# Kernel optimization log

Measured on AMD Instinct MI355X. Metric: run time of the kernel, lower is better.

Reference implementation:

```python
import jax, jax.numpy as jnp
from jax import lax
import numpy as np

D = 56      # latent_rep_size
H = 501     # GRU hidden size
T = 277     # repeat length (sequence length)
O = 76      # fc2 output


def setup_inputs() -> dict:
    key = jax.random.key(0)
    ks = jax.random.split(key, 20)
    B = 256
    s = 0.05
    inp = {"x": jax.random.normal(ks[0], (B, D), dtype=jnp.float32)}
    inp["fc1_w"] = jax.random.normal(ks[1], (D, D), dtype=jnp.float32) * s
    inp["fc1_b"] = jax.random.normal(ks[2], (D,), dtype=jnp.float32) * s
    k = 3
    for l, in_dim in enumerate([D, H, H]):
        inp[f"w_ih{l}"] = jax.random.normal(ks[k], (3 * H, in_dim), dtype=jnp.float32) * s; k += 1
        inp[f"w_hh{l}"] = jax.random.normal(ks[k], (3 * H, H), dtype=jnp.float32) * s; k += 1
        inp[f"b_ih{l}"] = jax.random.normal(ks[k], (3 * H,), dtype=jnp.float32) * s; k += 1
        inp[f"b_hh{l}"] = jax.random.normal(ks[k], (3 * H,), dtype=jnp.float32) * s; k += 1
    inp["fc2_w"] = jax.random.normal(ks[k], (O, H), dtype=jnp.float32) * s; k += 1
    inp["fc2_b"] = jax.random.normal(ks[k], (O,), dtype=jnp.float32) * s
    return inp


def _gru_step(h, g, w_hh, b_hh):
    # g: precomputed input gates (B, 3H) in PyTorch order [r, z, n]
    hg = h @ w_hh.T + b_hh                       # (B, 3H)
    r = jax.nn.sigmoid(g[:, :H] + hg[:, :H])
    z = jax.nn.sigmoid(g[:, H:2 * H] + hg[:, H:2 * H])
    n = jnp.tanh(g[:, 2 * H:] + r * hg[:, 2 * H:])
    h_new = (1.0 - z) * n + z * h
    return h_new, h_new


def _gru_layer(x_gates, w_hh, b_hh, B, dtype):
    # x_gates: (T, B, 3H) input contribution per timestep
    h0 = jnp.zeros((B, H), dtype)
    _, ys = lax.scan(lambda h, g: _gru_step(h, g, w_hh, b_hh), h0, x_gates)
    return ys  # (T, B, H)


def reference(x, fc1_w, fc1_b,
              w_ih0, w_hh0, b_ih0, b_hh0,
              w_ih1, w_hh1, b_ih1, b_hh1,
              w_ih2, w_hh2, b_ih2, b_hh2,
              fc2_w, fc2_b):
    B = x.shape[0]
    dtype = x.dtype
    # fc1 + relu, then the input is repeated 277 times -> layer-0 input gates
    # are identical at every timestep; compute them once (B, 3H).
    h_in = jax.nn.relu(x @ fc1_w.T + fc1_b)             # (B, D)
    g0 = h_in @ w_ih0.T + b_ih0                          # (B, 3H), constant over t
    h0 = jnp.zeros((B, H), dtype)
    _, ys0 = lax.scan(lambda h, _: _gru_step(h, g0, w_hh0, b_hh0), h0, None, length=T)
    # layers 1 and 2: precompute input gates for all timesteps, then scan
    g1 = jnp.einsum('tbh,gh->tbg', ys0, w_ih1) + b_ih1   # (T, B, 3H)
    ys1 = _gru_layer(g1, w_hh1, b_hh1, B, dtype)
    g2 = jnp.einsum('tbh,gh->tbg', ys1, w_ih2) + b_ih2
    ys2 = _gru_layer(g2, w_hh2, b_hh2, B, dtype)
    # fc2 then permute(1, 2, 0): (T, B, O) -> (B, O, T)
    out = jnp.einsum('tbh,oh->tbo', ys2, fc2_w) + fc2_b
    return jnp.transpose(out, (1, 2, 0))
```

## Files before the change

kernel.cpp:

```cpp
#include <hip/hip_runtime.h>
#include <hip/hip_bf16.h>
#include <math.h>

#define D_IN 56
#define H    501
#define T_STEPS 277
#define O_OUT 76
#define BATCH 256
#define HP   512
#define NP   1504
#define SSTR 520

#define LDS_SA    0
#define LDS_SB    (32 * SSTR)
#define LDS_SC    (64 * SSTR)
#define LDS_STAGE (96 * SSTR)
#define DYN_LDS   (96 * SSTR * 2 + 18 * 544 * 4 + 32 * 48 * 4 + 3 * 4 * 16 * 4)

typedef __attribute__((ext_vector_type(8))) short s16x8;
typedef __attribute__((ext_vector_type(4))) float f32x4;
typedef unsigned long long ull;

__device__ __forceinline__ short f2bf(float x) {
    union { float f; unsigned u; } v; v.f = x;
    unsigned r = (v.u + 0x7fffu + ((v.u >> 16) & 1u)) >> 16;
    return (short)r;
}
__device__ __forceinline__ float bf2f(short b) {
    union { unsigned u; float f; } v; v.u = ((unsigned)(unsigned short)b) << 16;
    return v.f;
}
__device__ __forceinline__ float sigm(float x) { return 1.f / (1.f + __expf(-x)); }
__device__ __forceinline__ float tanh_fast(float x) { return 1.f - 2.f / (1.f + __expf(2.f * x)); }

__global__ void k_pack_gru(const float* __restrict__ w_ih,
                           const float* __restrict__ w_hh,
                           short* __restrict__ dst, int KT) {
    int tile = blockIdx.x;
    int ktp  = tile % KT;
    int g    = (tile / KT) % 3;
    int j    = tile / (KT * 3);
    int l    = threadIdx.x;
    int u    = j * 16 + (l & 15);
    int row  = g * H + u;
    const float* src; int k0;
    if (KT == 32) {
        if (ktp < 16) { src = w_ih; k0 = ktp * 32; }
        else          { src = w_hh; k0 = (ktp - 16) * 32; }
    } else          { src = w_hh; k0 = ktp * 32; }
    k0 += (l >> 4) * 8;
    short* p = dst + ((size_t)tile * 64 + l) * 8;
    for (int jj = 0; jj < 8; jj++) {
        int k = k0 + jj;
        float v = 0.f;
        if (u < H && k < H) v = src[(size_t)row * H + k];
        p[jj] = f2bf(v);
    }
}

__global__ void k_pack_fc2(const float* __restrict__ w, short* __restrict__ dst) {
    int tile = blockIdx.x;
    int kt = tile % 16, mt = tile / 16;
    int l = threadIdx.x;
    int o = mt * 16 + (l & 15);
    int k0 = kt * 32 + (l >> 4) * 8;
    short* p = dst + ((size_t)tile * 64 + l) * 8;
    for (int jj = 0; jj < 8; jj++) {
        int k = k0 + jj; float v = 0.f;
        if (o < O_OUT && k < H) v = w[(size_t)o * H + k];
        p[jj] = f2bf(v);
    }
}

__global__ void k_hin(const float* __restrict__ x, const float* __restrict__ w,
                      const float* __restrict__ bias, float* __restrict__ hin) {
    int b = blockIdx.x, o = threadIdx.x;
    float acc = 0.f;
    if (o < D_IN) {
        acc = bias[o];
        for (int k = 0; k < D_IN; k++) acc += x[b * D_IN + k] * w[o * D_IN + k];
        acc = fmaxf(acc, 0.f);
    }
    hin[b * 64 + o] = (o < D_IN) ? acc : 0.f;
}

__global__ void k_g0(const float* __restrict__ hin, const float* __restrict__ w_ih0,
                     const float* __restrict__ b_ih0, float* __restrict__ g0) {
    int b = blockIdx.x, tid = threadIdx.x;
    __shared__ float shx[D_IN];
    if (tid < D_IN) shx[tid] = hin[b * 64 + tid];
    __syncthreads();
    for (int o = tid; o < NP; o += 256) {
        float acc = 0.f;
        if (o < 3 * H) {
            acc = b_ih0[o];
            for (int k = 0; k < D_IN; k++) acc += shx[k] * w_ih0[(size_t)o * D_IN + k];
        }
        g0[(size_t)b * NP + o] = acc;
    }
}

__global__ __launch_bounds__(384, 1)
void k_gru_persist(const short* __restrict__ packW0,
                   const short* __restrict__ packW1,
                   const short* __restrict__ packW2,
                   const float* __restrict__ g0,
                   const float* __restrict__ b_hh0,
                   const float* __restrict__ b_ih1, const float* __restrict__ b_hh1,
                   const float* __restrict__ b_ih2, const float* __restrict__ b_hh2,
                   short* __restrict__ ysA,
                   short* __restrict__ ysB,
                   unsigned* __restrict__ cnt) {
    const int bg   = blockIdx.x >> 5;
    const int j    = ((blockIdx.x & 7) << 2) | ((blockIdx.x >> 3) & 3);
    const int b0   = bg * 32;
    const int tid  = threadIdx.x;
    const int lane = tid & 63;
    const int wave = tid >> 6;
    const int nt   = wave >> 1;
    const int part = wave & 1;
    const int arow = lane & 15;
    const int acol = (lane >> 4) * 8;
    const s16x8 z8 = {0, 0, 0, 0, 0, 0, 0, 0};

    extern __shared__ __align__(16) char smem[];
    short* stg = (short*)smem;
    float* hgl = (float*)(smem + LDS_STAGE * 2);
    float* sg0 = hgl + 18 * 544;
    float* sbb = sg0 + 32 * 48;

    for (int c = tid; c < 32 * 48; c += 384) {
        int m = c / 48, col = c % 48;
        int g = col >> 4, ul = col & 15;
        int u = j * 16 + ul;
        float v = 0.f;
        if (u < H) {
            v = g0[(size_t)(b0 + m) * NP + g * H + u];
            if (g == 0) v += b_hh0[u];
            else if (g == 1) v += b_hh0[H + u];
        }
        sg0[m * 48 + col] = v;
    }
    if (tid < 48) {
        int l = tid >> 4, ul = tid & 15, u = j * 16 + ul;
        float br = 0.f, bz = 0.f, bxn = 0.f, bhn = 0.f;
        if (u < H) {
            if (l == 0) bhn = b_hh0[2 * H + u];
            else {
                const float* bi = (l == 1) ? b_ih1 : b_ih2;
                const float* bh = (l == 1) ? b_hh1 : b_hh2;
                br = bi[u] + bh[u]; bz = bi[H + u] + bh[H + u];
                bxn = bi[2 * H + u]; bhn = bh[2 * H + u];
            }
        }
        sbb[(l * 4 + 0) * 16 + ul] = br;  sbb[(l * 4 + 1) * 16 + ul] = bz;
        sbb[(l * 4 + 2) * 16 + ul] = bxn; sbb[(l * 4 + 3) * 16 + ul] = bhn;
    }
    __syncthreads();

    unsigned* mycnt = cnt + bg * 32;

    for (int s = 0; s < T_STEPS + 2; ++s) {
        const bool hasL0 = (s < T_STEPS);
        const bool hasL1 = (s >= 1 && s <= T_STEPS);
        const bool hasL2 = (s >= 2);
        const short* ysAm1 = ysA + (size_t)(s - 1) * BATCH * HP;
        const short* ysBm2 = ysB + (size_t)(s - 2) * BATCH * HP;
        const short* ysAm3 = ysA + (size_t)(s - 3) * BATCH * HP;

        #pragma unroll
        for (int i = 0; i < 6; i++) {
            int c = tid + i * 384;
            if (c < 2048) {
                int r = c >> 6, cc = c & 63;
                size_t goff = (size_t)(b0 + r) * HP + cc * 8;
                s16x8 va = z8, vb = z8, vc = z8;
                if (s >= 1 && s <= T_STEPS) va = *(const s16x8*)&ysAm1[goff];
                if (s >= 2)                 vb = *(const s16x8*)&ysBm2[goff];
                if (s >= 3) {
                    const ull* p = (const ull*)&ysAm3[goff];
                    union { ull q[2]; s16x8 v; } uu;
                    uu.q[0] = __hip_atomic_load(p,     __ATOMIC_RELAXED, __HIP_MEMORY_SCOPE_AGENT);
                    uu.q[1] = __hip_atomic_load(p + 1, __ATOMIC_RELAXED, __HIP_MEMORY_SCOPE_AGENT);
                    vc = uu.v;
                }
                int loff = r * SSTR + cc * 8;
                *(s16x8*)&stg[LDS_SA + loff] = va;
                *(s16x8*)&stg[LDS_SB + loff] = vb;
                *(s16x8*)&stg[LDS_SC + loff] = vc;
            }
        }
        __syncthreads();

        if (hasL0) {
            const short* wp = packW0 + (size_t)((j * 3 + nt) * 16 + part * 8) * 64 * 8;
            f32x4 a0 = {0.f,0.f,0.f,0.f}, a1 = {0.f,0.f,0.f,0.f};
            #pragma unroll
            for (int i = 0; i < 8; i++) {
                int kk = part * 8 + i;
                s16x8 bf = *(const s16x8*)&wp[((size_t)i * 64 + lane) * 8];
                s16x8 x0 = *(const s16x8*)&stg[LDS_SA + arow * SSTR + kk * 32 + acol];
                s16x8 x1 = *(const s16x8*)&stg[LDS_SA + (16 + arow) * SSTR + kk * 32 + acol];
                a0 = __builtin_amdgcn_mfma_f32_16x16x32_bf16(x0, bf, a0, 0, 0, 0);
                a1 = __builtin_amdgcn_mfma_f32_16x16x32_bf16(x1, bf, a1, 0, 0, 0);
            }
            float* d = hgl + (0 + nt * 2 + part) * 544;
            int ul = lane & 15, mrow = (lane >> 4) * 4;
            #pragma unroll
            for (int r = 0; r < 4; r++) {
                d[(mrow + r) * 17 + ul]      = a0[r];
                d[(16 + mrow + r) * 17 + ul] = a1[r];
            }
        }
        if (hasL1) {
            const short* wp = packW1 + (size_t)((j * 3 + nt) * 32 + part * 16) * 64 * 8;
            const int sbase = (part == 0) ? LDS_SA : LDS_SB;
            f32x4 a0 = {0.f,0.f,0.f,0.f}, a1 = {0.f,0.f,0.f,0.f};
            #pragma unroll
            for (int kk = 0; kk < 16; kk++) {
                s16x8 bf = *(const s16x8*)&wp[((size_t)kk * 64 + lane) * 8];
                s16x8 x0 = *(const s16x8*)&stg[sbase + arow * SSTR + kk * 32 + acol];
                s16x8 x1 = *(const s16x8*)&stg[sbase + (16 + arow) * SSTR + kk * 32 + acol];
                a0 = __builtin_amdgcn_mfma_f32_16x16x32_bf16(x0, bf, a0, 0, 0, 0);
                a1 = __builtin_amdgcn_mfma_f32_16x16x32_bf16(x1, bf, a1, 0, 0, 0);
            }
            float* d = hgl + (6 + nt * 2 + part) * 544;
            int ul = lane & 15, mrow = (lane >> 4) * 4;
            #pragma unroll
            for (int r = 0; r < 4; r++) {
                d[(mrow + r) * 17 + ul]      = a0[r];
                d[(16 + mrow + r) * 17 + ul] = a1[r];
            }
        }
        if (hasL2) {
            const short* wp = packW2 + (size_t)((j * 3 + nt) * 32 + part * 16) * 64 * 8;
            const int sbase = (part == 0) ? LDS_SB : LDS_SC;
            f32x4 a0 = {0.f,0.f,0.f,0.f}, a1 = {0.f,0.f,0.f,0.f};
            #pragma unroll
            for (int kk = 0; kk < 16; kk++) {
                s16x8 bf = *(const s16x8*)&wp[((size_t)kk * 64 + lane) * 8];
                s16x8 x0 = *(const s16x8*)&stg[sbase + arow * SSTR + kk * 32 + acol];
                s16x8 x1 = *(const s16x8*)&stg[sbase + (16 + arow) * SSTR + kk * 32 + acol];
                a0 = __builtin_amdgcn_mfma_f32_16x16x32_bf16(x0, bf, a0, 0, 0, 0);
                a1 = __builtin_amdgcn_mfma_f32_16x16x32_bf16(x1, bf, a1, 0, 0, 0);
            }
            float* d = hgl + (12 + nt * 2 + part) * 544;
            int ul = lane & 15, mrow = (lane >> 4) * 4;
            #pragma unroll
            for (int r = 0; r < 4; r++) {
                d[(mrow + r) * 17 + ul]      = a0[r];
                d[(16 + mrow + r) * 17 + ul] = a1[r];
            }
        }
        __syncthreads();

        #pragma unroll
        for (int it = 0; it < 2; it++) {
            int idx = tid + it * 384;
            int which = idx >> 8, id8 = idx & 255;
            int m = id8 >> 3, pr = id8 & 7;
            int b = b0 + m;
            if (which == 0 && hasL0) {
                short* dst = ysA + (size_t)s * BATCH * HP;
                unsigned pk = 0;
                #pragma unroll
                for (int e = 0; e < 2; e++) {
                    int ul = pr * 2 + e, u = j * 16 + ul, mo = m * 17 + ul;
                    float hv = 0.f;
                    if (u < H) {
                        float hr = hgl[0 * 544 + mo] + hgl[1 * 544 + mo];
                        float hz = hgl[2 * 544 + mo] + hgl[3 * 544 + mo];
                        float hn = hgl[4 * 544 + mo] + hgl[5 * 544 + mo];
                        float r = sigm(sg0[m * 48 + ul] + hr);
                        float z = sigm(sg0[m * 48 + 16 + ul] + hz);
                        float n = tanh_fast(sg0[m * 48 + 32 + ul] + r * (hn + sbb[3 * 16 + ul]));
                        float hold = bf2f(stg[LDS_SA + m * SSTR + u]);
                        hv = (1.f - z) * n + z * hold;
                    }
                    pk |= ((unsigned)(unsigned short)f2bf(hv)) << (16 * e);
                }
                __hip_atomic_store((unsigned*)&dst[(size_t)b * HP + j * 16 + pr * 2], pk,
                                   __ATOMIC_RELAXED, __HIP_MEMORY_SCOPE_AGENT);
            } else if (which == 1 && hasL1) {
                short* dst = ysB + (size_t)(s - 1) * BATCH * HP;
                unsigned pk = 0;
                #pragma unroll
                for (int e = 0; e < 2; e++) {
                    int ul = pr * 2 + e, u = j * 16 + ul, mo = m * 17 + ul;
                    float hv = 0.f;
                    if (u < H) {
                        float xr = hgl[6 * 544 + mo]  + sbb[(4 + 0) * 16 + ul];
                        float hr = hgl[7 * 544 + mo];
                        float xz = hgl[8 * 544 + mo]  + sbb[(4 + 1) * 16 + ul];
                        float hz = hgl[9 * 544 + mo];
                        float xn = hgl[10 * 544 + mo] + sbb[(4 + 2) * 16 + ul];
                        float hn = hgl[11 * 544 + mo] + sbb[(4 + 3) * 16 + ul];
                        float r = sigm(xr + hr);
                        float z = sigm(xz + hz);
                        float n = tanh_fast(xn + r * hn);
                        float hold = bf2f(stg[LDS_SB + m * SSTR + u]);
                        hv = (1.f - z) * n + z * hold;
                    }
                    pk |= ((unsigned)(unsigned short)f2bf(hv)) << (16 * e);
                }
                __hip_atomic_store((unsigned*)&dst[(size_t)b * HP + j * 16 + pr * 2], pk,
                                   __ATOMIC_RELAXED, __HIP_MEMORY_SCOPE_AGENT);
            } else if (which == 2 && hasL2) {
                short* dst = ysA + (size_t)(s - 2) * BATCH * HP;
                unsigned pk = 0;
                #pragma unroll
                for (int e = 0; e < 2; e++) {
                    int ul = pr * 2 + e, u = j * 16 + ul, mo = m * 17 + ul;
                    float hv = 0.f;
                    if (u < H) {
                        float xr = hgl[12 * 544 + mo] + sbb[(8 + 0) * 16 + ul];
                        float hr = hgl[13 * 544 + mo];
                        float xz = hgl[14 * 544 + mo] + sbb[(8 + 1) * 16 + ul];
                        float hz = hgl[15 * 544 + mo];
                        float xn = hgl[16 * 544 + mo] + sbb[(8 + 2) * 16 + ul];
                        float hn = hgl[17 * 544 + mo] + sbb[(8 + 3) * 16 + ul];
                        float r = sigm(xr + hr);
                        float z = sigm(xz + hz);
                        float n = tanh_fast(xn + r * hn);
                        float hold = bf2f(stg[LDS_SC + m * SSTR + u]);
                        hv = (1.f - z) * n + z * hold;
                    }
                    pk |= ((unsigned)(unsigned short)f2bf(hv)) << (16 * e);
                }
                __hip_atomic_store((unsigned*)&dst[(size_t)b * HP + j * 16 + pr * 2], pk,
                                   __ATOMIC_RELAXED, __HIP_MEMORY_SCOPE_AGENT);
            }
        }
        __syncthreads();

        if (tid == 0) {
            asm volatile("s_waitcnt vmcnt(0)" ::: "memory");
            __hip_atomic_fetch_add(mycnt, 1u, __ATOMIC_RELAXED, __HIP_MEMORY_SCOPE_AGENT);
            unsigned tgt = 32u * (unsigned)(s + 1);
            while (__hip_atomic_load(mycnt, __ATOMIC_RELAXED, __HIP_MEMORY_SCOPE_AGENT) < tgt) {}
        }
        __syncthreads();
    }
}

__global__ __launch_bounds__(256, 1)
void k_fc2(const short* __restrict__ ys2, const short* __restrict__ fc2p,
           const float* __restrict__ fc2_b, float* __restrict__ out) {
    int b = blockIdx.x;
    int tid = threadIdx.x, lane = tid & 63, wave = tid >> 6;
    const s16x8 zf = {0, 0, 0, 0, 0, 0, 0, 0};
    for (int ntile = wave; ntile < 18; ntile += 4) {
        int tt = ntile * 16 + (lane & 15);
        s16x8 bf[16];
        for (int kt = 0; kt < 16; kt++) {
            if (tt < T_STEPS)
                bf[kt] = *(const s16x8*)&ys2[((size_t)tt * BATCH + b) * HP + kt * 32 + (lane >> 4) * 8];
            else
                bf[kt] = zf;
        }
        for (int mt = 0; mt < 5; mt++) {
            f32x4 acc = {0.f, 0.f, 0.f, 0.f};
            for (int kt = 0; kt < 16; kt++) {
                s16x8 af = *(const s16x8*)&fc2p[(((size_t)mt * 16 + kt) * 64 + lane) * 8];
                acc = __builtin_amdgcn_mfma_f32_16x16x32_bf16(af, bf[kt], acc, 0, 0, 0);
            }
            int obase = mt * 16 + (lane >> 4) * 4;
            for (int r = 0; r < 4; r++) {
                int o = obase + r;
                if (o < O_OUT && tt < T_STEPS)
                    out[((size_t)b * O_OUT + o) * T_STEPS + tt] = acc[r] + fc2_b[o];
            }
        }
    }
}

extern "C" void kernel_launch(void* const* d_in, const int* in_sizes, int n_in,
                              void* d_out, int out_size, void* d_ws, size_t ws_size,
                              hipStream_t stream) {
    const float* x     = (const float*)d_in[0];
    const float* fc1_w = (const float*)d_in[1];
    const float* fc1_b = (const float*)d_in[2];
    const float* w_ih0 = (const float*)d_in[3];
    const float* w_hh0 = (const float*)d_in[4];
    const float* b_ih0 = (const float*)d_in[5];
    const float* b_hh0 = (const float*)d_in[6];
    const float* w_ih1 = (const float*)d_in[7];
    const float* w_hh1 = (const float*)d_in[8];
    const float* b_ih1 = (const float*)d_in[9];
    const float* b_hh1 = (const float*)d_in[10];
    const float* w_ih2 = (const float*)d_in[11];
    const float* w_hh2 = (const float*)d_in[12];
    const float* b_ih2 = (const float*)d_in[13];
    const float* b_hh2 = (const float*)d_in[14];
    const float* fc2_w = (const float*)d_in[15];
    const float* fc2_b = (const float*)d_in[16];
    float* out = (float*)d_out;

    char* p = (char*)d_ws;
    auto alloc = [&](size_t bytes) {
        char* r = p; p += (bytes + 255) & ~(size_t)255; return r;
    };
    short* packW0 = (short*)alloc((size_t)32 * 3 * 16 * 64 * 8 * 2);
    short* packW1 = (short*)alloc((size_t)32 * 3 * 32 * 64 * 8 * 2);
    short* packW2 = (short*)alloc((size_t)32 * 3 * 32 * 64 * 8 * 2);
    short* packF  = (short*)alloc((size_t)80 * 64 * 8 * 2);
    float* hin    = (float*)alloc((size_t)BATCH * 64 * 4);
    float* g0     = (float*)alloc((size_t)BATCH * NP * 4);
    unsigned* cnt = (unsigned*)alloc(256 * 4);
    short* ysA    = (short*)alloc((size_t)T_STEPS * BATCH * HP * 2);
    short* ysB    = (short*)alloc((size_t)T_STEPS * BATCH * HP * 2);

    static bool attr_set = false;
    if (!attr_set) {
        (void)hipFuncSetAttribute((const void*)k_gru_persist,
                                  hipFuncAttributeMaxDynamicSharedMemorySize,
                                  DYN_LDS);
        attr_set = true;
    }

    hipMemsetAsync(cnt, 0, 256 * 4, stream);
    k_pack_gru<<<32 * 3 * 16, 64, 0, stream>>>(nullptr, w_hh0, packW0, 16);
    k_pack_gru<<<32 * 3 * 32, 64, 0, stream>>>(w_ih1, w_hh1, packW1, 32);
    k_pack_gru<<<32 * 3 * 32, 64, 0, stream>>>(w_ih2, w_hh2, packW2, 32);
    k_pack_fc2<<<80, 64, 0, stream>>>(fc2_w, packF);
    k_hin<<<BATCH, 64, 0, stream>>>(x, fc1_w, fc1_b, hin);
    k_g0<<<BATCH, 256, 0, stream>>>(hin, w_ih0, b_ih0, g0);

    k_gru_persist<<<256, 384, DYN_LDS, stream>>>(packW0, packW1, packW2, g0,
                                                 b_hh0, b_ih1, b_hh1, b_ih2, b_hh2,
                                                 ysA, ysB, cnt);

    k_fc2<<<BATCH, 256, 0, stream>>>(ysA, packF, fc2_b, out);
}
```

Baseline: 2.472 ms.

## Assign each wave a single layer and K-half, computing all three gates

```diff
diff --git a/kernel.cpp b/kernel.cpp
--- a/kernel.cpp
+++ b/kernel.cpp
@@ -117,8 +117,6 @@
     const int tid  = threadIdx.x;
     const int lane = tid & 63;
     const int wave = tid >> 6;
-    const int nt   = wave >> 1;
-    const int part = wave & 1;
     const int arow = lane & 15;
     const int acol = (lane >> 4) * 8;
     const s16x8 z8 = {0, 0, 0, 0, 0, 0, 0, 0};
@@ -128,6 +126,20 @@
     float* hgl = (float*)(smem + LDS_STAGE * 2);
     float* sg0 = hgl + 18 * 544;
     float* sbb = sg0 + 32 * 48;
+
+    int layer, kt0, nk, abase, part; const short* wpk; int KT;
+    switch (wave) {
+        case 0:  layer = 0; kt0 = 0;  nk = 8;  abase = LDS_SA; wpk = packW0; KT = 16; part = 0; break;
+        case 1:  layer = 0; kt0 = 8;  nk = 8;  abase = LDS_SA; wpk = packW0; KT = 16; part = 1; break;
+        case 2:  layer = 1; kt0 = 0;  nk = 16; abase = LDS_SA; wpk = packW1; KT = 32; part = 0; break;
+        case 3:  layer = 1; kt0 = 16; nk = 16; abase = LDS_SB; wpk = packW1; KT = 32; part = 1; break;
+        case 4:  layer = 2; kt0 = 0;  nk = 16; abase = LDS_SB; wpk = packW2; KT = 32; part = 0; break;
+        default: layer = 2; kt0 = 16; nk = 16; abase = LDS_SC; wpk = packW2; KT = 32; part = 1; break;
+    }
+    const int aoff = (KT == 32 && part == 1) ? -16 : 0;
+    const short* wg0 = wpk + ((size_t)((j * 3 + 0) * KT + kt0) * 512);
+    const short* wg1 = wpk + ((size_t)((j * 3 + 1) * KT + kt0) * 512);
+    const short* wg2 = wpk + ((size_t)((j * 3 + 2) * KT + kt0) * 512);
 
     for (int c = tid; c < 32 * 48; c += 384) {
         int m = c / 48, col = c % 48;
@@ -192,64 +204,40 @@
         }
         __syncthreads();
 
-        if (hasL0) {
-            const short* wp = packW0 + (size_t)((j * 3 + nt) * 16 + part * 8) * 64 * 8;
-            f32x4 a0 = {0.f,0.f,0.f,0.f}, a1 = {0.f,0.f,0.f,0.f};
-            #pragma unroll
-            for (int i = 0; i < 8; i++) {
-                int kk = part * 8 + i;
-                s16x8 bf = *(const s16x8*)&wp[((size_t)i * 64 + lane) * 8];
-                s16x8 x0 = *(const s16x8*)&stg[LDS_SA + arow * SSTR + kk * 32 + acol];
-                s16x8 x1 = *(const s16x8*)&stg[LDS_SA + (16 + arow) * SSTR + kk * 32 + acol];
-                a0 = __builtin_amdgcn_mfma_f32_16x16x32_bf16(x0, bf, a0, 0, 0, 0);
-                a1 = __builtin_amdgcn_mfma_f32_16x16x32_bf16(x1, bf, a1, 0, 0, 0);
-            }
-            float* d = hgl + (0 + nt * 2 + part) * 544;
+        {
+            const bool active = (layer == 0) ? hasL0 : ((layer == 1) ? hasL1 : hasL2);
+            f32x4 ar0 = {0.f,0.f,0.f,0.f}, ar1 = {0.f,0.f,0.f,0.f};
+            f32x4 az0 = {0.f,0.f,0.f,0.f}, az1 = {0.f,0.f,0.f,0.f};
+            f32x4 an0 = {0.f,0.f,0.f,0.f}, an1 = {0.f,0.f,0.f,0.f};
+            if (active) {
+                #pragma unroll 4
+                for (int kk = 0; kk < nk; kk++) {
+                    int ak = kt0 + kk + aoff;
+                    s16x8 x0 = *(const s16x8*)&stg[abase + arow * SSTR + ak * 32 + acol];
+                    s16x8 x1 = *(const s16x8*)&stg[abase + (16 + arow) * SSTR + ak * 32 + acol];
+                    s16x8 br = *(const s16x8*)&wg0[(size_t)kk * 512 + lane * 8];
+                    s16x8 bz = *(const s16x8*)&wg1[(size_t)kk * 512 + lane * 8];
+                    s16x8 bn = *(const s16x8*)&wg2[(size_t)kk * 512 + lane * 8];
+                    ar0 = __builtin_amdgcn_mfma_f32_16x16x32_bf16(x0, br, ar0, 0, 0, 0);
+                    ar1 = __builtin_amdgcn_mfma_f32_16x16x32_bf16(x1, br, ar1, 0, 0, 0);
+                    az0 = __builtin_amdgcn_mfma_f32_16x16x32_bf16(x0, bz, az0, 0, 0, 0);
+                    az1 = __builtin_amdgcn_mfma_f32_16x16x32_bf16(x1, bz, az1, 0, 0, 0);
+                    an0 = __builtin_amdgcn_mfma_f32_16x16x32_bf16(x0, bn, an0, 0, 0, 0);
+                    an1 = __builtin_amdgcn_mfma_f32_16x16x32_bf16(x1, bn, an1, 0, 0, 0);
+                }
+            }
             int ul = lane & 15, mrow = (lane >> 4) * 4;
+            float* dr = hgl + (layer * 6 + 0 * 2 + part) * 544;
+            float* dz = hgl + (layer * 6 + 1 * 2 + part) * 544;
+            float* dn = hgl + (layer * 6 + 2 * 2 + part) * 544;
             #pragma unroll
             for (int r = 0; r < 4; r++) {
-                d[(mrow + r) * 17 + ul]      = a0[r];
-                d[(16 + mrow + r) * 17 + ul] = a1[r];
-            }
-        }
-        if (hasL1) {
-            const short* wp = packW1 + (size_t)((j * 3 + nt) * 32 + part * 16) * 64 * 8;
-            const int sbase = (part == 0) ? LDS_SA : LDS_SB;
-            f32x4 a0 = {0.f,0.f,0.f,0.f}, a1 = {0.f,0.f,0.f,0.f};
-            #pragma unroll
-            for (int kk = 0; kk < 16; kk++) {
-                s16x8 bf = *(const s16x8*)&wp[((size_t)kk * 64 + lane) * 8];
-                s16x8 x0 = *(const s16x8*)&stg[sbase + arow * SSTR + kk * 32 + acol];
-                s16x8 x1 = *(const s16x8*)&stg[sbase + (16 + arow) * SSTR + kk * 32 + acol];
-                a0 = __builtin_amdgcn_mfma_f32_16x16x32_bf16(x0, bf, a0, 0, 0, 0);
-                a1 = __builtin_amdgcn_mfma_f32_16x16x32_bf16(x1, bf, a1, 0, 0, 0);
-            }
-            float* d = hgl + (6 + nt * 2 + part) * 544;
-            int ul = lane & 15, mrow = (lane >> 4) * 4;
-            #pragma unroll
-            for (int r = 0; r < 4; r++) {
-                d[(mrow + r) * 17 + ul]      = a0[r];
-                d[(16 + mrow + r) * 17 + ul] = a1[r];
-            }
-        }
-        if (hasL2) {
-            const short* wp = packW2 + (size_t)((j * 3 + nt) * 32 + part * 16) * 64 * 8;
-            const int sbase = (part == 0) ? LDS_SB : LDS_SC;
-            f32x4 a0 = {0.f,0.f,0.f,0.f}, a1 = {0.f,0.f,0.f,0.f};
-            #pragma unroll
-            for (int kk = 0; kk < 16; kk++) {
-                s16x8 bf = *(const s16x8*)&wp[((size_t)kk * 64 + lane) * 8];
-                s16x8 x0 = *(const s16x8*)&stg[sbase + arow * SSTR + kk * 32 + acol];
-                s16x8 x1 = *(const s16x8*)&stg[sbase + (16 + arow) * SSTR + kk * 32 + acol];
-                a0 = __builtin_amdgcn_mfma_f32_16x16x32_bf16(x0, bf, a0, 0, 0, 0);
-                a1 = __builtin_amdgcn_mfma_f32_16x16x32_bf16(x1, bf, a1, 0, 0, 0);
-            }
-            float* d = hgl + (12 + nt * 2 + part) * 544;
-            int ul = lane & 15, mrow = (lane >> 4) * 4;
-            #pragma unroll
-            for (int r = 0; r < 4; r++) {
-                d[(mrow + r) * 17 + ul]      = a0[r];
-                d[(16 + mrow + r) * 17 + ul] = a1[r];
+                dr[(mrow + r) * 17 + ul]      = ar0[r];
+                dr[(16 + mrow + r) * 17 + ul] = ar1[r];
+                dz[(mrow + r) * 17 + ul]      = az0[r];
+                dz[(16 + mrow + r) * 17 + ul] = az1[r];
+                dn[(mrow + r) * 17 + ul]      = an0[r];
+                dn[(16 + mrow + r) * 17 + ul] = an1[r];
             }
         }
         __syncthreads();
```

Result: slower. 3.526 ms (+42.6%).
